# Optimization experiments

Hardware: AMD Instinct MI355X
Metric: run time of the kernel (lower is better)

Reference implementation:

```python
import jax, jax.numpy as jnp
import numpy as np

B = 32768
K = 4096  # num_embeddings
D = 512   # embedding_dim
COMMITMENT_COST = 0.25


def setup_inputs() -> dict:
    key = jax.random.key(0)
    k1, k2 = jax.random.split(key)
    inputs = jax.random.normal(k1, (B, D), dtype=jnp.float32)
    # nn.Embedding weight init: uniform(-1/K, 1/K)
    codebook = jax.random.uniform(k2, (K, D), dtype=jnp.float32,
                                  minval=-1.0 / K, maxval=1.0 / K)
    return {"inputs": inputs, "codebook": codebook}


def reference(inputs, codebook):
    distances = (jnp.sum(inputs ** 2, axis=1, keepdims=True)
                 + jnp.sum(codebook ** 2, axis=1)
                 - 2.0 * jnp.matmul(inputs, codebook.T))
    encoding_indices = jnp.argmin(distances, axis=1)  # [B]
    # one-hot encodings are part of the module's returned dict
    encodings = jax.nn.one_hot(encoding_indices, K, dtype=inputs.dtype)  # [B, K]
    # quantized = encodings @ codebook == direct gather (same math)
    quantized = codebook[encoding_indices]  # [B, D]

    sg = jax.lax.stop_gradient
    e_latent_loss = jnp.mean((sg(quantized) - inputs) ** 2)
    q_latent_loss = jnp.mean((quantized - sg(inputs)) ** 2)
    loss = q_latent_loss + COMMITMENT_COST * e_latent_loss

    # straight-through estimator
    quantized_st = inputs + sg(quantized - inputs)

    avg_probs = jnp.mean(encodings, axis=0)  # [K]
    perplexity = jnp.exp(-jnp.sum(avg_probs * jnp.log(avg_probs + 1e-10)))

    return quantized_st, encoding_indices, loss, perplexity, encodings
```

## Files before the change

### kernel.cpp

```cpp
#include <hip/hip_runtime.h>
#include <hip/hip_bf16.h>


typedef __attribute__((ext_vector_type(8))) short bf16x8;
typedef __attribute__((ext_vector_type(4))) float f32x4;

#define BB 32768
#define KK 4096
#define DD 512

#define IDX_OFF  (BB*DD)
#define LOSS_OFF (IDX_OFF + BB)
#define PERP_OFF (LOSS_OFF + 1)
#define ENC_OFF  (PERP_OFF + 1)

#define WSB_XSQ  0
#define WSB_ESQ  131072
#define WSB_IDX  147456
#define WSB_HIST 278528
#define WSB_LOSS 294912
#define WSB_EBF2 294928
#define WSB_XBF  4489232
#define WSB_PART 38043664

#define MARG 2.5e-4f
#define NCAND 16

static __device__ __forceinline__ unsigned short f2bf(float f) {
    __hip_bfloat16 h = __float2bfloat16(f);
    return *reinterpret_cast<unsigned short*>(&h);
}

static __device__ __forceinline__ unsigned int packscore(float s, int col) {
    unsigned int u = __float_as_uint(s);
    u ^= (u & 0x80000000u) ? 0xFFFFFFFFu : 0x80000000u;
    return (u & 0xFFFFF000u) | (unsigned int)col;
}
static __device__ __forceinline__ float unpackscore(unsigned int p) {
    unsigned int u = p & 0xFFFFF000u;
    u = (u & 0x80000000u) ? (u ^ 0x80000000u) : ~u;
    return __uint_as_float(u);
}

static __device__ __forceinline__ void gll16(const void* g, void* l) {
    __builtin_amdgcn_global_load_lds(
        (const __attribute__((address_space(1))) unsigned int*)g,
        (__attribute__((address_space(3))) unsigned int*)l, 16, 0, 0);
}

__global__ __launch_bounds__(256) void init_kernel(int* __restrict__ hist,
                                                   double* __restrict__ loss_acc) {
    int i = blockIdx.x * 256 + threadIdx.x;
    if (i < KK) hist[i] = 0;
    if (i == 0) *loss_acc = 0.0;
}

__global__ __launch_bounds__(256) void npsum_pack_kernel(const float* __restrict__ X,
                                                         const float* __restrict__ E,
                                                         float* __restrict__ xsq,
                                                         float* __restrict__ esq,
                                                         unsigned short* __restrict__ Xbf) {
    __shared__ float sq[4][512];
    __shared__ float ub[4][64];
    __shared__ float bb[4][4];
    int w = threadIdx.x >> 6, lane = threadIdx.x & 63;
    int row = blockIdx.x * 4 + w;
    const float* src; float* dst;
    bool isx = (row < BB);
    if (isx) { src = X + (size_t)row * DD;        dst = xsq + row; }
    else     { src = E + (size_t)(row - BB) * DD; dst = esq + (row - BB); }
    const float4* s4 = (const float4*)(src + lane * 8);
    float4 a = s4[0], b = s4[1];
    sq[w][lane * 8 + 0] = __fmul_rn(a.x, a.x);
    sq[w][lane * 8 + 1] = __fmul_rn(a.y, a.y);
    sq[w][lane * 8 + 2] = __fmul_rn(a.z, a.z);
    sq[w][lane * 8 + 3] = __fmul_rn(a.w, a.w);
    sq[w][lane * 8 + 4] = __fmul_rn(b.x, b.x);
    sq[w][lane * 8 + 5] = __fmul_rn(b.y, b.y);
    sq[w][lane * 8 + 6] = __fmul_rn(b.z, b.z);
    sq[w][lane * 8 + 7] = __fmul_rn(b.w, b.w);
    if (isx) {
        int kt64 = lane >> 3, ks = (lane >> 2) & 1, oct = lane & 3;
        int rf = (row >> 4) & 15;
        size_t unit = ((size_t)((row >> 8) * 8 + kt64)) * 2048
                    + (size_t)((rf * 2 + ks) * 64 + oct * 16 + (row & 15));
        union { bf16x8 v; unsigned short us[8]; } pk;
        pk.us[0] = f2bf(a.x); pk.us[1] = f2bf(a.y); pk.us[2] = f2bf(a.z); pk.us[3] = f2bf(a.w);
        pk.us[4] = f2bf(b.x); pk.us[5] = f2bf(b.y); pk.us[6] = f2bf(b.z); pk.us[7] = f2bf(b.w);
        *(bf16x8*)(Xbf + unit * 8) = pk.v;
    }
    __syncthreads();
    {
        int b2 = lane >> 4, l = lane & 15;
        const float* s = &sq[w][b2 * 128];
        float t = __fadd_rn(
            __fadd_rn(__fadd_rn(s[l], s[16 + l]), __fadd_rn(s[32 + l], s[48 + l])),
            __fadd_rn(__fadd_rn(s[64 + l], s[80 + l]), __fadd_rn(s[96 + l], s[112 + l])));
        ub[w][lane] = t;
    }
    __syncthreads();
    if (lane < 4) {
        const float* u = &ub[w][lane * 16];
        float T3[8], T6[4];
        #pragma unroll
        for (int i = 0; i < 8; ++i) T3[i] = __fadd_rn(u[i], u[i + 8]);
        #pragma unroll
        for (int i = 0; i < 4; ++i) T6[i] = __fadd_rn(T3[i], T3[i + 4]);
        bb[w][lane] = __fadd_rn(__fadd_rn(T6[0], T6[2]), __fadd_rn(T6[1], T6[3]));
    }
    __syncthreads();
    if (lane == 0)
        *dst = __fadd_rn(__fadd_rn(bb[w][0], bb[w][1]), __fadd_rn(bb[w][2], bb[w][3]));
}

__global__ __launch_bounds__(256) void packE_kernel(const float* __restrict__ src,
                                                    unsigned short* __restrict__ dst) {
    int t = blockIdx.x * 256 + threadIdx.x;
    int chunk = t >> 11, u = t & 2047;
    int rb2 = chunk >> 3, kt = chunk & 7;
    int rf = u >> 7, ks = (u >> 6) & 1, lane = u & 63;
    int row = rb2 * 256 + rf * 16 + (lane & 15);
    int k   = kt * 64 + ks * 32 + (lane >> 4) * 8;
    const float4* s = (const float4*)(src + (size_t)row * DD + k);
    float4 a = s[0], b = s[1];
    union { bf16x8 v; unsigned short us[8]; } pk;
    pk.us[0] = f2bf(a.x); pk.us[1] = f2bf(a.y); pk.us[2] = f2bf(a.z); pk.us[3] = f2bf(a.w);
    pk.us[4] = f2bf(b.x); pk.us[5] = f2bf(b.y); pk.us[6] = f2bf(b.z); pk.us[7] = f2bf(b.w);
    *(bf16x8*)(dst + (size_t)t * 8) = pk.v;
}

__global__ __launch_bounds__(256, 4) void gemm_screen(
    const unsigned short* __restrict__ Xbf, const unsigned short* __restrict__ Ebf2,
    const float* __restrict__ esqw, uint2* __restrict__ partials)
{
    __shared__ __align__(16) char pool[32768];

    const int tid = threadIdx.x;
    const int w = tid >> 6, lane = tid & 63;
    const int c = lane & 15, g = lane >> 4;
    const int bid = blockIdx.x;
    const int orig = (bid & 7) * 1024 + (bid >> 3);
    const int rb = orig >> 5, cb = orig & 31;
    const int row0 = rb * 128, col0 = cb * 128;
    const int mw = w >> 1, nw = w & 1;

    const int hA = rb & 1, hB = cb & 1;
    const char* Xc = (const char*)Xbf  + (size_t)(rb >> 1) * 8 * 32768;
    const char* Ec = (const char*)Ebf2 + (size_t)(cb >> 1) * 8 * 32768;

    f32x4 acc[4][4];
    #pragma unroll
    for (int i = 0; i < 4; ++i)
        #pragma unroll
        for (int j = 0; j < 4; ++j) acc[i][j] = (f32x4){0.f, 0.f, 0.f, 0.f};

    #define STAGE(srcc_, h_, kt_, dstoff_) { \
        const char* sb_ = (srcc_) + (size_t)((kt_) >> 1) * 32768; \
        const int ks_ = (kt_) & 1; \
        _Pragma("unroll") for (int it_ = 0; it_ < 2; ++it_) { \
            const char* s_ = sb_ + (size_t)((((h_) * 8 + it_ * 4 + w) * 2 + ks_) * 64 + lane) * 16; \
            char* d_ = pool + (dstoff_) + (it_ * 4 + w) * 1024; \
            gll16(s_, d_); } }

    STAGE(Xc, hA, 0, 0); STAGE(Ec, hB, 0, 16384);
    __syncthreads();
    int buf = 0;
    for (int kt = 0; kt < 16; ++kt) {
        if (kt < 15) {
            STAGE(Xc, hA, kt + 1, (buf ^ 1) * 8192);
            STAGE(Ec, hB, kt + 1, 16384 + (buf ^ 1) * 8192);
        }
        const char* Ap = pool + buf * 8192;
        const char* Bp = pool + 16384 + buf * 8192;
        bf16x8 af[4], bfr[4];
        #pragma unroll
        for (int i = 0; i < 4; ++i) {
            af[i]  = *(const bf16x8*)(Ap + (((mw * 4 + i) * 64) + lane) * 16);
            bfr[i] = *(const bf16x8*)(Bp + (((nw * 4 + i) * 64) + lane) * 16);
        }
        #pragma unroll
        for (int mf = 0; mf < 4; ++mf)
            #pragma unroll
            for (int nf = 0; nf < 4; ++nf)
                acc[mf][nf] = __builtin_amdgcn_mfma_f32_16x16x32_bf16(af[mf], bfr[nf], acc[mf][nf], 0, 0, 0);
        __syncthreads();
        buf ^= 1;
    }

    uint2* P = (uint2*)pool;
    #pragma unroll
    for (int mf = 0; mf < 4; ++mf) {
        #pragma unroll
        for (int r = 0; r < 4; ++r) {
            unsigned int q1 = 0xFFFFFFFFu, q2 = 0xFFFFFFFFu;
            int rowl = mw * 64 + mf * 16 + g * 4 + r;
            #pragma unroll
            for (int nf = 0; nf < 4; ++nf) {
                int col = col0 + nw * 64 + nf * 16 + c;
                float s = fmaf(-2.0f, acc[mf][nf][r], esqw[col]);
                unsigned int q = packscore(s, col);
                if (q < q1) { q2 = q1; q1 = q; } else if (q < q2) q2 = q;
            }
            P[(nw * 128 + rowl) * 16 + c] = make_uint2(q1, q2);
        }
    }
    __syncthreads();
    if (tid < 128) {
        int row = tid;
        #pragma unroll
        for (int n2 = 0; n2 < 2; ++n2) {
            unsigned int m1 = 0xFFFFFFFFu, m2 = 0xFFFFFFFFu;
            #pragma unroll 4
            for (int cc = 0; cc < 16; ++cc) {
                uint2 e = P[(n2 * 128 + row) * 16 + cc];
                if (e.x < m1) { m2 = m1; m1 = e.x; } else if (e.x < m2) m2 = e.x;
                if (e.y < m1) { m2 = m1; m1 = e.y; } else if (e.y < m2) m2 = e.y;
            }
            partials[(size_t)(cb * 2 + n2) * BB + row0 + row] = make_uint2(m1, m2);
        }
    }
    #undef STAGE
}

__global__ __launch_bounds__(256) void reduce_kernel(
    const float* __restrict__ X, const float* __restrict__ E,
    const float* __restrict__ xsqw, const float* __restrict__ esqw,
    const uint2* __restrict__ partials, int* __restrict__ idxbuf,
    int* __restrict__ hist, double* __restrict__ loss_acc,
    float* __restrict__ out)
{
    __shared__ double lred[256];
    const int row = blockIdx.x * 256 + threadIdx.x;
    unsigned int m = 0xFFFFFFFFu;
    for (int e = 0; e < 64; ++e) m = min(m, partials[(size_t)e * BB + row].x);
    float lim = unpackscore(m) + MARG;
    int cand[NCAND]; int nc = 0;
    for (int e = 0; e < 64; ++e) {
        uint2 p = partials[(size_t)e * BB + row];
        if (unpackscore(p.x) <= lim && nc < NCAND) cand[nc++] = (int)(p.x & 0xFFFu);
        if (unpackscore(p.y) <= lim && nc < NCAND) cand[nc++] = (int)(p.y & 0xFFFu);
    }
    const float* xr = X + (size_t)row * DD;
    float xs = xsqw[row];
    float bd = 3.0e38f; int bk = 0x7fffffff;
    for (int cidx = 0; cidx < nc; ++cidx) {
        int k = cand[cidx] & (KK - 1);
        const float* er = E + (size_t)k * DD;
        float q1 = 0.f, q2 = 0.f;
        for (int d = 0; d < 384; ++d)   q1 = fmaf(xr[d], er[d], q1);
        for (int d = 384; d < 512; ++d) q2 = fmaf(xr[d], er[d], q2);
        float dot = __fadd_rn(q1, q2);
        float t1  = __fadd_rn(xs, esqw[k]);
        float dnp = __fsub_rn(t1, __fmul_rn(2.0f, dot));
        if (dnp < bd || (dnp == bd && k < bk)) { bd = dnp; bk = k; }
    }
    const float* er = E + (size_t)bk * DD;
    double ls = 0.0;
    for (int d = 0; d < DD; ++d) {
        double df = (double)xr[d] - (double)er[d];
        ls = fma(df, df, ls);
    }
    idxbuf[row] = bk;
    out[IDX_OFF + row] = (float)bk;
    atomicAdd(&hist[bk], 1);
    lred[threadIdx.x] = ls;
    __syncthreads();
    for (int t = 128; t > 0; t >>= 1) {
        if (threadIdx.x < t) lred[threadIdx.x] += lred[threadIdx.x + t];
        __syncthreads();
    }
    if (threadIdx.x == 0) atomicAdd(loss_acc, lred[0]);
}

__global__ __launch_bounds__(256) void encq_kernel(const int* __restrict__ idxbuf,
                                                   const float* __restrict__ E,
                                                   float* __restrict__ out) {
    int row = blockIdx.x;
    int idx = idxbuf[row];
    ((float2*)out)[(size_t)row * 256 + threadIdx.x] =
        ((const float2*)E)[(size_t)idx * 256 + threadIdx.x];
    float2* erow = (float2*)(out + ENC_OFF) + (size_t)row * (KK / 2);
    int half = idx >> 1;
    float2 one;
    if (idx & 1) { one.x = 0.f; one.y = 1.f; } else { one.x = 1.f; one.y = 0.f; }
    float2 z; z.x = 0.f; z.y = 0.f;
    for (int c = threadIdx.x; c < KK / 2; c += 256)
        erow[c] = (c == half) ? one : z;
}

__global__ __launch_bounds__(256) void fin_kernel(const int* __restrict__ hist,
                                                  const double* __restrict__ loss_acc,
                                                  float* __restrict__ out) {
    __shared__ double red[256];
    int tid = threadIdx.x;
    double s = 0.0;
    for (int k = tid; k < KK; k += 256) {
        double p = (double)hist[k] * (1.0 / 32768.0);
        s += p * log(p + 1e-10);
    }
    red[tid] = s;
    __syncthreads();
    for (int t = 128; t > 0; t >>= 1) {
        if (tid < t) red[tid] += red[tid + t];
        __syncthreads();
    }
    if (tid == 0) {
        double perp = exp(-red[0]);
        double L = loss_acc[0] * (1.0 / ((double)BB * (double)DD));
        out[LOSS_OFF] = (float)(1.25 * L);
        out[PERP_OFF] = (float)perp;
    }
}

extern "C" void kernel_launch(void* const* d_in, const int* in_sizes, int n_in,
                              void* d_out, int out_size, void* d_ws, size_t ws_size,
                              hipStream_t stream) {
    const float* X; const float* E;
    if (in_sizes[0] == BB * DD) { X = (const float*)d_in[0]; E = (const float*)d_in[1]; }
    else                        { X = (const float*)d_in[1]; E = (const float*)d_in[0]; }
    float* out = (float*)d_out;

    float* xsq = (float*)((char*)d_ws + WSB_XSQ);
    float* esq = (float*)((char*)d_ws + WSB_ESQ);
    int* idxbuf = (int*)((char*)d_ws + WSB_IDX);
    int* hist   = (int*)((char*)d_ws + WSB_HIST);
    double* loss_acc = (double*)((char*)d_ws + WSB_LOSS);
    unsigned short* Ebf2 = (unsigned short*)((char*)d_ws + WSB_EBF2);
    unsigned short* Xbf  = (unsigned short*)((char*)d_ws + WSB_XBF);
    uint2* partials = (uint2*)((char*)d_ws + WSB_PART);

    hipLaunchKernelGGL(init_kernel, dim3(16), dim3(256), 0, stream, hist, loss_acc);
    hipLaunchKernelGGL(npsum_pack_kernel, dim3((BB + KK) / 4), dim3(256), 0, stream,
                       X, E, xsq, esq, Xbf);
    hipLaunchKernelGGL(packE_kernel, dim3(1024), dim3(256), 0, stream, E, Ebf2);
    hipLaunchKernelGGL(gemm_screen, dim3(8192), dim3(256), 0, stream,
                       Xbf, Ebf2, esq, partials);
    hipLaunchKernelGGL(reduce_kernel, dim3(BB / 256), dim3(256), 0, stream,
                       X, E, xsq, esq, partials, idxbuf, hist, loss_acc, out);
    hipLaunchKernelGGL(encq_kernel, dim3(BB), dim3(256), 0, stream, idxbuf, E, out);
    hipLaunchKernelGGL(fin_kernel, dim3(1), dim3(256), 0, stream, hist, loss_acc, out);
}
```

Baseline: 458.4 us.

## Keep a full codebook slab in LDS, stream X fragments from global, shuffle-reduce top-2

The screening GEMM now uses 128x64 tiles. The whole 64-column by 512-K bf16 codebook slab is loaded into 64KB of LDS once per block, and A fragments are read straight from global memory inside a fully unrolled K loop, which removes the per-step double-buffer barriers. The per-row top-2 merge now uses wave shuffles instead of an LDS scratch pass and second barrier. The hist and loss zeroing moves into the codebook pack kernel, removing one launch. In exchange the grid doubles, so X is re-read from L2 twice as often, and occupancy drops to two blocks per CU with no explicit prefetch of A.

```diff
diff --git a/kernel.cpp b/kernel.cpp
--- a/kernel.cpp
+++ b/kernel.cpp
@@ -19,7 +19,7 @@
 #define WSB_IDX  147456
 #define WSB_HIST 278528
 #define WSB_LOSS 294912
-#define WSB_EBF2 294928
+#define WSB_EBF3 294928
 #define WSB_XBF  4489232
 #define WSB_PART 38043664
 
@@ -46,13 +46,6 @@
     __builtin_amdgcn_global_load_lds(
         (const __attribute__((address_space(1))) unsigned int*)g,
         (__attribute__((address_space(3))) unsigned int*)l, 16, 0, 0);
-}
-
-__global__ __launch_bounds__(256) void init_kernel(int* __restrict__ hist,
-                                                   double* __restrict__ loss_acc) {
-    int i = blockIdx.x * 256 + threadIdx.x;
-    if (i < KK) hist[i] = 0;
-    if (i == 0) *loss_acc = 0.0;
 }
 
 __global__ __launch_bounds__(256) void npsum_pack_kernel(const float* __restrict__ X,
@@ -113,113 +106,101 @@
         *dst = __fadd_rn(__fadd_rn(bb[w][0], bb[w][1]), __fadd_rn(bb[w][2], bb[w][3]));
 }
 
-__global__ __launch_bounds__(256) void packE_kernel(const float* __restrict__ src,
-                                                    unsigned short* __restrict__ dst) {
+__global__ __launch_bounds__(256) void packE3_kernel(const float* __restrict__ E,
+                                                     unsigned short* __restrict__ Ebf3,
+                                                     int* __restrict__ hist,
+                                                     double* __restrict__ loss_acc) {
     int t = blockIdx.x * 256 + threadIdx.x;
-    int chunk = t >> 11, u = t & 2047;
-    int rb2 = chunk >> 3, kt = chunk & 7;
-    int rf = u >> 7, ks = (u >> 6) & 1, lane = u & 63;
-    int row = rb2 * 256 + rf * 16 + (lane & 15);
-    int k   = kt * 64 + ks * 32 + (lane >> 4) * 8;
-    const float4* s = (const float4*)(src + (size_t)row * DD + k);
+    if (t < KK) hist[t] = 0;
+    if (t == KK) *loss_acc = 0.0;
+    int cbb = t >> 12, u = t & 4095;
+    int ks = u >> 8, nf = (u >> 6) & 3, lane = u & 63;
+    int col = cbb * 64 + nf * 16 + (lane & 15);
+    int k   = ks * 32 + (lane >> 4) * 8;
+    const float4* s = (const float4*)(E + (size_t)col * DD + k);
     float4 a = s[0], b = s[1];
     union { bf16x8 v; unsigned short us[8]; } pk;
     pk.us[0] = f2bf(a.x); pk.us[1] = f2bf(a.y); pk.us[2] = f2bf(a.z); pk.us[3] = f2bf(a.w);
     pk.us[4] = f2bf(b.x); pk.us[5] = f2bf(b.y); pk.us[6] = f2bf(b.z); pk.us[7] = f2bf(b.w);
-    *(bf16x8*)(dst + (size_t)t * 8) = pk.v;
-}
-
-__global__ __launch_bounds__(256, 4) void gemm_screen(
-    const unsigned short* __restrict__ Xbf, const unsigned short* __restrict__ Ebf2,
+    *(bf16x8*)(Ebf3 + (size_t)t * 8) = pk.v;
+}
+
+__global__ __launch_bounds__(256, 2) void gemm_screen(
+    const unsigned short* __restrict__ Xbf, const unsigned short* __restrict__ Ebf3,
     const float* __restrict__ esqw, uint2* __restrict__ partials)
 {
-    __shared__ __align__(16) char pool[32768];
+    __shared__ __align__(16) char Bsh[65536];
 
     const int tid = threadIdx.x;
     const int w = tid >> 6, lane = tid & 63;
     const int c = lane & 15, g = lane >> 4;
     const int bid = blockIdx.x;
-    const int orig = (bid & 7) * 1024 + (bid >> 3);
-    const int rb = orig >> 5, cb = orig & 31;
-    const int row0 = rb * 128, col0 = cb * 128;
-    const int mw = w >> 1, nw = w & 1;
-
-    const int hA = rb & 1, hB = cb & 1;
-    const char* Xc = (const char*)Xbf  + (size_t)(rb >> 1) * 8 * 32768;
-    const char* Ec = (const char*)Ebf2 + (size_t)(cb >> 1) * 8 * 32768;
-
-    f32x4 acc[4][4];
+    const int orig = (bid & 7) * 2048 + (bid >> 3);
+    const int rb = orig >> 6, cbb = orig & 63;
+    const int row0 = rb * 128, col0 = cbb * 64;
+
+    {
+        const char* src = (const char*)Ebf3 + (size_t)cbb * 65536 + (size_t)tid * 16;
+        char* dst = Bsh + w * 1024;
+        #pragma unroll
+        for (int j = 0; j < 16; ++j)
+            gll16(src + j * 4096, dst + j * 4096);
+    }
+
+    const char* Xc = (const char*)Xbf + (size_t)(rb >> 1) * 262144;
+    const int rfb = (rb & 1) * 8 + w * 2;
+
+    f32x4 acc[2][4];
     #pragma unroll
-    for (int i = 0; i < 4; ++i)
+    for (int i = 0; i < 2; ++i)
         #pragma unroll
         for (int j = 0; j < 4; ++j) acc[i][j] = (f32x4){0.f, 0.f, 0.f, 0.f};
 
-    #define STAGE(srcc_, h_, kt_, dstoff_) { \
-        const char* sb_ = (srcc_) + (size_t)((kt_) >> 1) * 32768; \
-        const int ks_ = (kt_) & 1; \
-        _Pragma("unroll") for (int it_ = 0; it_ < 2; ++it_) { \
-            const char* s_ = sb_ + (size_t)((((h_) * 8 + it_ * 4 + w) * 2 + ks_) * 64 + lane) * 16; \
-            char* d_ = pool + (dstoff_) + (it_ * 4 + w) * 1024; \
-            gll16(s_, d_); } }
-
-    STAGE(Xc, hA, 0, 0); STAGE(Ec, hB, 0, 16384);
-    __syncthreads();
-    int buf = 0;
-    for (int kt = 0; kt < 16; ++kt) {
-        if (kt < 15) {
-            STAGE(Xc, hA, kt + 1, (buf ^ 1) * 8192);
-            STAGE(Ec, hB, kt + 1, 16384 + (buf ^ 1) * 8192);
+    __syncthreads();
+
+    #pragma unroll
+    for (int ks = 0; ks < 16; ++ks) {
+        const size_t base = (size_t)(ks >> 1) * 32768 + (size_t)(ks & 1) * 1024
+                          + (size_t)lane * 16;
+        bf16x8 a0 = *(const bf16x8*)(Xc + base + (size_t)(rfb + 0) * 2048);
+        bf16x8 a1 = *(const bf16x8*)(Xc + base + (size_t)(rfb + 1) * 2048);
+        #pragma unroll
+        for (int nf = 0; nf < 4; ++nf) {
+            bf16x8 b = *(const bf16x8*)(Bsh + (((ks * 4 + nf) * 64) + lane) * 16);
+            acc[0][nf] = __builtin_amdgcn_mfma_f32_16x16x32_bf16(a0, b, acc[0][nf], 0, 0, 0);
+            acc[1][nf] = __builtin_amdgcn_mfma_f32_16x16x32_bf16(a1, b, acc[1][nf], 0, 0, 0);
         }
-        const char* Ap = pool + buf * 8192;
-        const char* Bp = pool + 16384 + buf * 8192;
-        bf16x8 af[4], bfr[4];
-        #pragma unroll
-        for (int i = 0; i < 4; ++i) {
-            af[i]  = *(const bf16x8*)(Ap + (((mw * 4 + i) * 64) + lane) * 16);
-            bfr[i] = *(const bf16x8*)(Bp + (((nw * 4 + i) * 64) + lane) * 16);
-        }
-        #pragma unroll
-        for (int mf = 0; mf < 4; ++mf)
-            #pragma unroll
-            for (int nf = 0; nf < 4; ++nf)
-                acc[mf][nf] = __builtin_amdgcn_mfma_f32_16x16x32_bf16(af[mf], bfr[nf], acc[mf][nf], 0, 0, 0);
-        __syncthreads();
-        buf ^= 1;
-    }
-
-    uint2* P = (uint2*)pool;
+    }
+
+    float es[4];
     #pragma unroll
-    for (int mf = 0; mf < 4; ++mf) {
+    for (int nf = 0; nf < 4; ++nf) es[nf] = esqw[col0 + nf * 16 + c];
+    #pragma unroll
+    for (int mf = 0; mf < 2; ++mf) {
         #pragma unroll
         for (int r = 0; r < 4; ++r) {
             unsigned int q1 = 0xFFFFFFFFu, q2 = 0xFFFFFFFFu;
-            int rowl = mw * 64 + mf * 16 + g * 4 + r;
             #pragma unroll
             for (int nf = 0; nf < 4; ++nf) {
-                int col = col0 + nw * 64 + nf * 16 + c;
-                float s = fmaf(-2.0f, acc[mf][nf][r], esqw[col]);
+                int col = col0 + nf * 16 + c;
+                float s = fmaf(-2.0f, acc[mf][nf][r], es[nf]);
                 unsigned int q = packscore(s, col);
                 if (q < q1) { q2 = q1; q1 = q; } else if (q < q2) q2 = q;
             }
-            P[(nw * 128 + rowl) * 16 + c] = make_uint2(q1, q2);
+            #pragma unroll
+            for (int off = 1; off < 16; off <<= 1) {
+                unsigned int o1 = (unsigned int)__shfl_xor((int)q1, off, 64);
+                unsigned int o2 = (unsigned int)__shfl_xor((int)q2, off, 64);
+                unsigned int n1 = min(q1, o1);
+                unsigned int n2 = min(max(q1, o1), min(q2, o2));
+                q1 = n1; q2 = n2;
+            }
+            if (c == 0) {
+                int row = row0 + w * 32 + mf * 16 + g * 4 + r;
+                partials[(size_t)cbb * BB + row] = make_uint2(q1, q2);
+            }
         }
     }
-    __syncthreads();
-    if (tid < 128) {
-        int row = tid;
-        #pragma unroll
-        for (int n2 = 0; n2 < 2; ++n2) {
-            unsigned int m1 = 0xFFFFFFFFu, m2 = 0xFFFFFFFFu;
-            #pragma unroll 4
-            for (int cc = 0; cc < 16; ++cc) {
-                uint2 e = P[(n2 * 128 + row) * 16 + cc];
-                if (e.x < m1) { m2 = m1; m1 = e.x; } else if (e.x < m2) m2 = e.x;
-                if (e.y < m1) { m2 = m1; m1 = e.y; } else if (e.y < m2) m2 = e.y;
-            }
-            partials[(size_t)(cb * 2 + n2) * BB + row0 + row] = make_uint2(m1, m2);
-        }
-    }
-    #undef STAGE
 }
 
 __global__ __launch_bounds__(256) void reduce_kernel(
@@ -325,16 +306,16 @@
     int* idxbuf = (int*)((char*)d_ws + WSB_IDX);
     int* hist   = (int*)((char*)d_ws + WSB_HIST);
     double* loss_acc = (double*)((char*)d_ws + WSB_LOSS);
-    unsigned short* Ebf2 = (unsigned short*)((char*)d_ws + WSB_EBF2);
+    unsigned short* Ebf3 = (unsigned short*)((char*)d_ws + WSB_EBF3);
     unsigned short* Xbf  = (unsigned short*)((char*)d_ws + WSB_XBF);
     uint2* partials = (uint2*)((char*)d_ws + WSB_PART);
 
-    hipLaunchKernelGGL(init_kernel, dim3(16), dim3(256), 0, stream, hist, loss_acc);
     hipLaunchKernelGGL(npsum_pack_kernel, dim3((BB + KK) / 4), dim3(256), 0, stream,
                        X, E, xsq, esq, Xbf);
-    hipLaunchKernelGGL(packE_kernel, dim3(1024), dim3(256), 0, stream, E, Ebf2);
-    hipLaunchKernelGGL(gemm_screen, dim3(8192), dim3(256), 0, stream,
-                       Xbf, Ebf2, esq, partials);
+    hipLaunchKernelGGL(packE3_kernel, dim3(1024), dim3(256), 0, stream,
+                       E, Ebf3, hist, loss_acc);
+    hipLaunchKernelGGL(gemm_screen, dim3(16384), dim3(256), 0, stream,
+                       Xbf, Ebf3, esq, partials);
     hipLaunchKernelGGL(reduce_kernel, dim3(BB / 256), dim3(256), 0, stream,
                        X, E, xsq, esq, partials, idxbuf, hist, loss_acc, out);
     hipLaunchKernelGGL(encq_kernel, dim3(BB), dim3(256), 0, stream, idxbuf, E, out);
```

After: 535.8 us. 1.17x slower.

## Zero one-hot encodings inside GEMM epilogue and fold init into packE

Applied to the files above, without the earlier changes.

The full zero-fill of the 512 MB one-hot encodings output moves from encq_kernel into the end of each gemm_screen block. The aim is to overlap these streaming writes with the GEMM's compute-heavy work. encq_kernel now only copies the quantized row and writes the single 1.0 entry. The separate init kernel is removed: its histogram and loss-accumulator zeroing is folded into packE_kernel, saving one launch. The added stores may compete with the GEMM's memory traffic and raise register or occupancy pressure in its epilogue.

```diff
diff --git a/kernel.cpp b/kernel.cpp
--- a/kernel.cpp
+++ b/kernel.cpp
@@ -46,13 +46,6 @@
     __builtin_amdgcn_global_load_lds(
         (const __attribute__((address_space(1))) unsigned int*)g,
         (__attribute__((address_space(3))) unsigned int*)l, 16, 0, 0);
-}
-
-__global__ __launch_bounds__(256) void init_kernel(int* __restrict__ hist,
-                                                   double* __restrict__ loss_acc) {
-    int i = blockIdx.x * 256 + threadIdx.x;
-    if (i < KK) hist[i] = 0;
-    if (i == 0) *loss_acc = 0.0;
 }
 
 __global__ __launch_bounds__(256) void npsum_pack_kernel(const float* __restrict__ X,
@@ -114,8 +107,12 @@
 }
 
 __global__ __launch_bounds__(256) void packE_kernel(const float* __restrict__ src,
-                                                    unsigned short* __restrict__ dst) {
+                                                    unsigned short* __restrict__ dst,
+                                                    int* __restrict__ hist,
+                                                    double* __restrict__ loss_acc) {
     int t = blockIdx.x * 256 + threadIdx.x;
+    if (t < KK) hist[t] = 0;
+    if (t == KK) *loss_acc = 0.0;
     int chunk = t >> 11, u = t & 2047;
     int rb2 = chunk >> 3, kt = chunk & 7;
     int rf = u >> 7, ks = (u >> 6) & 1, lane = u & 63;
@@ -131,7 +128,8 @@
 
 __global__ __launch_bounds__(256, 4) void gemm_screen(
     const unsigned short* __restrict__ Xbf, const unsigned short* __restrict__ Ebf2,
-    const float* __restrict__ esqw, uint2* __restrict__ partials)
+    const float* __restrict__ esqw, uint2* __restrict__ partials,
+    float* __restrict__ out)
 {
     __shared__ __align__(16) char pool[32768];
 
@@ -218,6 +216,12 @@
             }
             partials[(size_t)(cb * 2 + n2) * BB + row0 + row] = make_uint2(m1, m2);
         }
+    }
+    {
+        float2* z = (float2*)(out + ENC_OFF) + (size_t)bid * 8192;
+        float2 zz; zz.x = 0.f; zz.y = 0.f;
+        #pragma unroll
+        for (int j = 0; j < 32; ++j) z[tid + j * 256] = zz;
     }
     #undef STAGE
 }
@@ -279,13 +283,11 @@
     int idx = idxbuf[row];
     ((float2*)out)[(size_t)row * 256 + threadIdx.x] =
         ((const float2*)E)[(size_t)idx * 256 + threadIdx.x];
-    float2* erow = (float2*)(out + ENC_OFF) + (size_t)row * (KK / 2);
-    int half = idx >> 1;
-    float2 one;
-    if (idx & 1) { one.x = 0.f; one.y = 1.f; } else { one.x = 1.f; one.y = 0.f; }
-    float2 z; z.x = 0.f; z.y = 0.f;
-    for (int c = threadIdx.x; c < KK / 2; c += 256)
-        erow[c] = (c == half) ? one : z;
+    if (threadIdx.x == 0) {
+        float2 one;
+        if (idx & 1) { one.x = 0.f; one.y = 1.f; } else { one.x = 1.f; one.y = 0.f; }
+        ((float2*)(out + ENC_OFF))[(size_t)row * (KK / 2) + (idx >> 1)] = one;
+    }
 }
 
 __global__ __launch_bounds__(256) void fin_kernel(const int* __restrict__ hist,
@@ -329,12 +331,12 @@
     unsigned short* Xbf  = (unsigned short*)((char*)d_ws + WSB_XBF);
     uint2* partials = (uint2*)((char*)d_ws + WSB_PART);
 
-    hipLaunchKernelGGL(init_kernel, dim3(16), dim3(256), 0, stream, hist, loss_acc);
     hipLaunchKernelGGL(npsum_pack_kernel, dim3((BB + KK) / 4), dim3(256), 0, stream,
                        X, E, xsq, esq, Xbf);
-    hipLaunchKernelGGL(packE_kernel, dim3(1024), dim3(256), 0, stream, E, Ebf2);
+    hipLaunchKernelGGL(packE_kernel, dim3(1024), dim3(256), 0, stream,
+                       E, Ebf2, hist, loss_acc);
     hipLaunchKernelGGL(gemm_screen, dim3(8192), dim3(256), 0, stream,
-                       Xbf, Ebf2, esq, partials);
+                       Xbf, Ebf2, esq, partials, out);
     hipLaunchKernelGGL(reduce_kernel, dim3(BB / 256), dim3(256), 0, stream,
                        X, E, xsq, esq, partials, idxbuf, hist, loss_acc, out);
     hipLaunchKernelGGL(encq_kernel, dim3(BB), dim3(256), 0, stream, idxbuf, E, out);
```

New measurement: 479.8 us. +4.7%, slower.
